# Kernel optimization log

Hardware: AMD Instinct MI355X
Metric: run time of the kernel (lower is better)

Reference implementation:

```python
import jax, jax.numpy as jnp
import numpy as np

B, S, DIM = 4, 2048, 768
H, HD, QK, R = 12, 64, 32, 8  # nheads, head_dim, qk_dim, nrules
EPS = 1e-5


def _ln(x, g, b):
    m = jnp.mean(x, axis=-1, keepdims=True)
    v = jnp.mean((x - m) ** 2, axis=-1, keepdims=True)
    return (x - m) / jnp.sqrt(v + EPS) * g + b


def setup_inputs() -> dict:
    key = jax.random.key(0)
    ks = jax.random.split(key, 12)
    w = lambda k, sh: (jax.random.normal(k, sh, jnp.float32) * 0.02)
    return {
        "x": jax.random.normal(ks[0], (B, S, DIM), jnp.float32),
        "Wq": w(ks[1], (DIM, DIM)), "bq": jnp.zeros((DIM,), jnp.float32),
        "Wk": w(ks[2], (DIM, DIM)), "bk": jnp.zeros((DIM,), jnp.float32),
        "Wv": w(ks[3], (DIM, HD * R)), "bv": jnp.zeros((HD * R,), jnp.float32),
        "Wqv": w(ks[4], (DIM, QK * H)), "bqv": jnp.zeros((QK * H,), jnp.float32),
        "Ws": w(ks[5], (QK + HD, 1)), "bs": jnp.zeros((1,), jnp.float32),
        "Wf": w(ks[6], (DIM, DIM)), "bf": jnp.zeros((DIM,), jnp.float32),
        "W1": w(ks[7], (DIM, 2 * DIM)), "b1": jnp.zeros((2 * DIM,), jnp.float32),
        "W2": w(ks[8], (2 * DIM, DIM)), "b2": jnp.zeros((DIM,), jnp.float32),
        "g1": jnp.ones((DIM,), jnp.float32), "be1": jnp.zeros((DIM,), jnp.float32),
        "g2": jnp.ones((DIM,), jnp.float32), "be2": jnp.zeros((DIM,), jnp.float32),
    }


def reference(x, Wq, bq, Wk, bk, Wv, bv, Wqv, bqv, Ws, bs, Wf, bf,
              W1, b1, W2, b2, g1, be1, g2, be2):
    b, n, _ = x.shape
    res = x
    xn = _ln(x, g1, be1)  # norm_before=True

    # --- stage 1: standard per-head attention, shared across rules ---
    q = (xn @ Wq + bq).reshape(b, n, H, HD) / np.sqrt(HD)
    k = (xn @ Wk + bk).reshape(b, n, H, HD)
    v = (xn @ Wv + bv).reshape(b, n, R, HD)
    score = jax.nn.softmax(jnp.einsum("bqhd,bkhd->bhqk", q, k), axis=-1)
    out = jnp.einsum("bhqk,bkrd->bqhrd", score, v)  # [B,S,H,R,hd]

    # --- stage 2: rule composition via score_network (dot=False) ---
    qv = (xn @ Wqv + bqv).reshape(b, n, H, QK) / np.sqrt(QK)
    # score_network(cat(q_v, out)) == q_v @ Ws[:QK] + out @ Ws[QK:] + bs
    ws_q, ws_o = Ws[:QK, 0], Ws[QK:, 0]
    comp = (jnp.einsum("bqhrd,d->bqhr", out, ws_o)
            + jnp.einsum("bqhk,k->bqh", qv, ws_q)[..., None] + bs[0])
    prev = comp[..., None]  # [B,S,H,R,1] raw scores, returned as `prev`

    rule_w = jax.nn.softmax(comp, axis=-1)  # softmax over rules
    o = jnp.einsum("bqhr,bqhrd->bqhd", rule_w, out).reshape(b, n, DIM)
    o = o @ Wf + bf

    out1 = res + o
    # post-block MLP (dropout inactive at inference)
    on = _ln(out1, g2, be2)
    mlp = jax.nn.relu(on @ W1 + b1) @ W2 + b2
    return out1 + mlp, prev
```

## Files before the change

kernel.cpp:

```cpp
#include <hip/hip_runtime.h>
#include <hip/hip_bf16.h>

typedef __bf16 bfrag  __attribute__((ext_vector_type(8)));
typedef __bf16 bf16x4 __attribute__((ext_vector_type(4)));
typedef float  f32x4  __attribute__((ext_vector_type(4)));

#define MFMA(a,b,c) __builtin_amdgcn_mfma_f32_16x16x32_bf16(a,b,c,0,0,0)

__device__ __forceinline__ void gl_lds16(const void* g, void* l) {
  __builtin_amdgcn_global_load_lds((const __attribute__((address_space(1))) void*)g,
                                   (__attribute__((address_space(3))) void*)l, 16, 0, 0);
}
__device__ __forceinline__ float fexp2(float x) {
  float r;
  asm("v_exp_f32 %0, %1" : "=v"(r) : "v"(x));
  return r;
}
__device__ __forceinline__ unsigned cvtpk(float lo, float hi) {
  unsigned r;
  asm("v_cvt_pk_bf16_f32 %0, %1, %2" : "=v"(r) : "v"(lo), "v"(hi));
  return r;
}

#define NC 2432

#define OFF_C     ((size_t)0)
#define OFF_VT    ((size_t)52428800)
#define OFF_QDOT  ((size_t)61079552)
#define OFF_WCAT  ((size_t)61472768)
#define OFF_BCAT  ((size_t)65208320)
#define OFF_WFT   ((size_t)65218048)
#define OFF_W1T   ((size_t)66397696)
#define OFF_W2T   ((size_t)68756992)
#define OFF_ATTNO ((size_t)71116288)
#define OFF_XN    ((size_t)39845888)
#define OFF_OUT1  ((size_t)0)
#define OFF_ON    ((size_t)12582912)
#define OFF_H1    ((size_t)25165824)

template<typename TIN>
__global__ __launch_bounds__(256) void k_ln(const TIN* __restrict__ in,
    const float* __restrict__ g, const float* __restrict__ be, __bf16* __restrict__ out) {
  int row  = blockIdx.x * 4 + (threadIdx.x >> 6);
  int lane = threadIdx.x & 63;
  const TIN* rp = in + (size_t)row * 768;
  float v[12];
  #pragma unroll
  for (int i = 0; i < 3; i++) {
    int c = i * 256 + lane * 4;
    if constexpr (sizeof(TIN) == 4) {
      float4 lv = *(const float4*)(rp + c);
      v[i*4+0] = lv.x; v[i*4+1] = lv.y; v[i*4+2] = lv.z; v[i*4+3] = lv.w;
    } else {
      bf16x4 lv = *(const bf16x4*)(rp + c);
      #pragma unroll
      for (int jj = 0; jj < 4; jj++) v[i*4+jj] = (float)lv[jj];
    }
  }
  float s = 0.f, sq = 0.f;
  #pragma unroll
  for (int k = 0; k < 12; k++) { s += v[k]; sq += v[k]*v[k]; }
  #pragma unroll
  for (int d = 1; d < 64; d <<= 1) { s += __shfl_xor(s, d); sq += __shfl_xor(sq, d); }
  float mean = s * (1.f/768.f);
  float rstd = rsqrtf(sq * (1.f/768.f) - mean*mean + 1e-5f);
  #pragma unroll
  for (int i = 0; i < 3; i++) {
    int c = i * 256 + lane * 4;
    float4 gv = *(const float4*)(g + c);
    float4 bv = *(const float4*)(be + c);
    bf16x4 o;
    o[0] = (__bf16)((v[i*4+0]-mean)*rstd*gv.x + bv.x);
    o[1] = (__bf16)((v[i*4+1]-mean)*rstd*gv.y + bv.y);
    o[2] = (__bf16)((v[i*4+2]-mean)*rstd*gv.z + bv.z);
    o[3] = (__bf16)((v[i*4+3]-mean)*rstd*gv.w + bv.w);
    *(bf16x4*)(out + (size_t)row*768 + c) = o;
  }
}

__global__ __launch_bounds__(256) void k_packT(const float* __restrict__ src, __bf16* __restrict__ dst,
                                               int N, int K, int total) {
  int idx = blockIdx.x * 256 + threadIdx.x;
  if (idx >= total) return;
  int K8 = K >> 3;
  int n = idx / K8, k0 = (idx % K8) * 8;
  bfrag o;
  #pragma unroll
  for (int i = 0; i < 8; i++) o[i] = (__bf16)src[(size_t)(k0+i)*N + n];
  *(bfrag*)&dst[(size_t)n*K + k0] = o;
}

__global__ __launch_bounds__(256) void k_packcat(
    const float* __restrict__ Wq, const float* __restrict__ Wk,
    const float* __restrict__ Wv, const float* __restrict__ Wqv,
    const float* __restrict__ bq, const float* __restrict__ bk,
    const float* __restrict__ bv, const float* __restrict__ bqv,
    __bf16* __restrict__ Wt, float* __restrict__ bcat) {
  int idx = blockIdx.x * 256 + threadIdx.x;
  if (idx >= 2432 * 96) return;
  int n = idx / 96, k0 = (idx % 96) * 8;
  const float* src; int col, sN; float sc = 1.f;
  if (n < 768)       { src = Wq;  col = n;        sN = 768; sc = 0.125f; }
  else if (n < 1536) { src = Wk;  col = n - 768;  sN = 768; }
  else if (n < 2048) { src = Wv;  col = n - 1536; sN = 512; }
  else               { src = Wqv; col = n - 2048; sN = 384; sc = 0.1767766952966369f; }
  bfrag o;
  #pragma unroll
  for (int i = 0; i < 8; i++) o[i] = (__bf16)(src[(size_t)(k0+i)*sN + col] * sc);
  *(bfrag*)&Wt[(size_t)n*768 + k0] = o;
  if (k0 == 0) {
    float bb;
    if (n < 768) bb = bq[col]*0.125f;
    else if (n < 1536) bb = bk[col];
    else if (n < 2048) bb = bv[col];
    else bb = bqv[col]*0.1767766952966369f;
    bcat[n] = bb;
  }
}

template<int KD, int EPI>
__global__ __launch_bounds__(256, 3) void k_gemm(const __bf16* __restrict__ A,
    const __bf16* __restrict__ Bt, const float* __restrict__ bias,
    const float* __restrict__ resf, const __bf16* __restrict__ resb,
    void* __restrict__ Cout, int N) {
  __shared__ __bf16 Al[2][128*32];
  __shared__ __bf16 Bl[2][128*32];
  const int bx = (blockIdx.x & 7) * 8 + (blockIdx.x >> 3);
  const int m0 = bx * 128, n0 = blockIdx.y * 128;
  const int tid = threadIdx.x, lane = tid & 63, w = tid >> 6;
  const int wm = (w >> 1) * 64, wn = (w & 1) * 64;
  const int srow = lane >> 2, skoff = (lane & 3) * 8;
  const int l15 = lane & 15, lg = lane >> 4;
  f32x4 acc[4][4];
  #pragma unroll
  for (int i = 0; i < 4; i++)
    #pragma unroll
    for (int j = 0; j < 4; j++) acc[i][j] = (f32x4){0.f,0.f,0.f,0.f};
  const int NT = KD / 32;
  auto stage = [&](int buf, int k0) {
    #pragma unroll
    for (int i = 0; i < 2; i++) {
      int c = w * 2 + i;
      gl_lds16(A  + (size_t)(m0 + c*16 + srow) * KD + k0 + skoff, &Al[buf][c*512]);
      gl_lds16(Bt + (size_t)(n0 + c*16 + srow) * KD + k0 + skoff, &Bl[buf][c*512]);
    }
  };
  stage(0, 0);
  __syncthreads();
  for (int t = 0; t < NT; t++) {
    int buf = t & 1;
    if (t + 1 < NT) stage(buf ^ 1, (t + 1) * 32);
    bfrag af[4], bfm[4];
    #pragma unroll
    for (int f = 0; f < 4; f++) {
      af[f]  = *(const bfrag*)&Al[buf][(wm + f*16 + l15)*32 + lg*8];
      bfm[f] = *(const bfrag*)&Bl[buf][(wn + f*16 + l15)*32 + lg*8];
    }
    #pragma unroll
    for (int i = 0; i < 4; i++)
      #pragma unroll
      for (int j = 0; j < 4; j++)
        acc[i][j] = MFMA(af[i], bfm[j], acc[i][j]);
    __syncthreads();
  }
  #pragma unroll
  for (int i = 0; i < 4; i++) {
    int row0 = m0 + wm + i*16 + lg*4;
    #pragma unroll
    for (int j = 0; j < 4; j++) {
      int col = n0 + wn + j*16 + l15;
      float bv = bias[col];
      #pragma unroll
      for (int q = 0; q < 4; q++) {
        size_t r = (size_t)(row0 + q);
        float v = acc[i][j][q] + bv;
        if (EPI == 0)      ((__bf16*)Cout)[r*N + col] = (__bf16)v;
        else if (EPI == 1) { v += resf[r*N + col]; ((__bf16*)Cout)[r*N + col] = (__bf16)v; }
        else if (EPI == 2) ((__bf16*)Cout)[r*N + col] = (__bf16)fmaxf(v, 0.f);
        else               { v += (float)resb[r*N + col]; ((float*)Cout)[r*N + col] = v; }
      }
    }
  }
}

__global__ __launch_bounds__(256) void k_vt(const __bf16* __restrict__ C, __bf16* __restrict__ VT) {
  int bid = blockIdx.x;
  int b = bid >> 8, dt = (bid >> 5) & 7, kt = bid & 31;
  __shared__ __bf16 tile[64][72];
  int tid = threadIdx.x;
  int r = tid >> 3, c0 = (tid & 7) * 8;
  #pragma unroll
  for (int p = 0; p < 2; p++) {
    int rr = r + p * 32;
    bfrag v = *(const bfrag*)&C[(size_t)(b*2048 + kt*64 + rr)*NC + 1536 + dt*64 + c0];
    *(bfrag*)&tile[rr][c0] = v;
  }
  __syncthreads();
  #pragma unroll
  for (int p = 0; p < 2; p++) {
    int d = r + p * 32;
    bfrag o;
    #pragma unroll
    for (int i = 0; i < 8; i++) o[i] = tile[c0 + i][d];
    *(bfrag*)&VT[((size_t)b*512 + dt*64 + d)*2048 + kt*64 + c0] = o;
  }
}

__global__ __launch_bounds__(256) void k_qdot(const __bf16* __restrict__ C, const float* __restrict__ Ws,
                                              const float* __restrict__ bs, float* __restrict__ qd) {
  int idx = blockIdx.x * 256 + threadIdx.x;
  if (idx >= 98304) return;
  int h = idx % 12; size_t srow = (size_t)(idx / 12);
  const __bf16* qp = &C[srow*NC + 2048 + h*32];
  float s = bs[0];
  #pragma unroll
  for (int j = 0; j < 32; j++) s += (float)qp[j] * Ws[j];
  qd[idx] = s;
}

__global__ __launch_bounds__(512, 2) void k_attn(const __bf16* __restrict__ C,
    const __bf16* __restrict__ VT, const float* __restrict__ Ws,
    const float* __restrict__ qdot, __bf16* __restrict__ attno, float* __restrict__ prevout) {
  __shared__ __align__(16) char smem[53248];
  __bf16* Pl   = (__bf16*)(smem);
  __bf16* kbuf = (__bf16*)(smem + 32768);
  float*  wlb  = (float*)(smem + 49152);
  __bf16* rbuf = (__bf16*)(smem);

  const int tid = threadIdx.x, lane = tid & 63, wid = tid >> 6;
  const int l15 = lane & 15, lg = lane >> 4;
  const int bid = (blockIdx.x & 7) * 96 + (blockIdx.x >> 3);
  const int b = bid / 192, rem = bid % 192, h = rem / 16, qb = rem % 16;
  const int q0 = qb * 128;

  const __bf16* VTb = VT + (size_t)b * 512 * 2048;
  const int kkey = tid >> 3, kch = tid & 7;
  const __bf16* Ksrc0 = C + (size_t)(b*2048 + kkey)*NC + 768 + h*64 + ((kch ^ (kkey & 7)) * 8);

  auto stageK = [&](int t) {
    gl_lds16(Ksrc0 + (size_t)t * 64 * NC, kbuf + (t & 1)*4096 + (size_t)wid*512);
  };
  stageK(0);

  const __bf16* Qbase = C + (size_t)(b*2048 + q0 + wid*16 + l15)*NC + h*64 + lg*8;
  bfrag qf0 = *(const bfrag*)(Qbase);
  bfrag qf1 = *(const bfrag*)(Qbase + 32);

  f32x4 accv[8][4];
  #pragma unroll
  for (int i = 0; i < 8; i++)
    #pragma unroll
    for (int j = 0; j < 4; j++) accv[i][j] = (f32x4){0.f,0.f,0.f,0.f};
  float lsc = 0.f;

  auto qk_phase = [&](int tn) {
    const __bf16* kb_ = kbuf + (tn & 1) * 4096;
    f32x4 s[4];
    #pragma unroll
    for (int cf = 0; cf < 4; cf++) s[cf] = (f32x4){0.f,0.f,0.f,0.f};
    #pragma unroll
    for (int cf = 0; cf < 4; cf++) {
      int key = cf*16 + l15, swz = key & 7;
      bfrag ka  = *(const bfrag*)(kb_ + key*64 + ((lg     ^ swz) * 8));
      bfrag kb2 = *(const bfrag*)(kb_ + key*64 + (((lg+4) ^ swz) * 8));
      s[cf] = MFMA(ka, qf0, s[cf]);
      s[cf] = MFMA(kb2, qf1, s[cf]);
    }
    int row = wid*16 + l15;
    char* base = (char*)Pl + (tn & 1)*16384 + row*128;
    int swz = (row & 7) << 4;
    #pragma unroll
    for (int cf = 0; cf < 4; cf++) {
      float p0 = fexp2(s[cf][0] * 1.44269504f);
      float p1 = fexp2(s[cf][1] * 1.44269504f);
      float p2 = fexp2(s[cf][2] * 1.44269504f);
      float p3 = fexp2(s[cf][3] * 1.44269504f);
      lsc += (p0 + p1) + (p2 + p3);
      uint2 pk;
      pk.x = cvtpk(p0, p1);
      pk.y = cvtpk(p2, p3);
      *(uint2*)(base + ((cf*32 + lg*8) ^ swz)) = pk;
    }
  };

  __syncthreads();

  qk_phase(0);
  stageK(1);

  for (int t = 0; t < 32; t++) {
    const int k0 = t * 64, pb = t & 1;
    __syncthreads();
    if (t + 2 < 32) stageK(t + 2);
    bfrag vb[4][2];
    #pragma unroll
    for (int cf = 0; cf < 4; cf++) {
      const __bf16* vp = VTb + (size_t)(wid*64 + cf*16 + l15)*2048 + k0 + lg*8;
      vb[cf][0] = *(const bfrag*)(vp);
      vb[cf][1] = *(const bfrag*)(vp + 32);
    }
    if (t < 31) qk_phase(t + 1);
    __builtin_amdgcn_s_setprio(1);
    #pragma unroll
    for (int rf = 0; rf < 8; rf++) {
      int prow = rf*16 + l15;
      int swz = (prow & 7) << 4;
      const char* pbase = (const char*)Pl + pb*16384 + prow*128;
      bfrag pa0 = *(const bfrag*)(pbase + ((lg*16) ^ swz));
      bfrag pa1 = *(const bfrag*)(pbase + ((64 + lg*16) ^ swz));
      #pragma unroll
      for (int cf = 0; cf < 4; cf++) {
        accv[rf][cf] = MFMA(pa0, vb[cf][0], accv[rf][cf]);
        accv[rf][cf] = MFMA(pa1, vb[cf][1], accv[rf][cf]);
      }
    }
    __builtin_amdgcn_s_setprio(0);
  }
  float lfall = lsc;
  lfall += __shfl_xor(lfall, 16);
  lfall += __shfl_xor(lfall, 32);
  float lf[4];
  #pragma unroll
  for (int j = 0; j < 4; j++) lf[j] = __shfl(lfall, lg*4 + j);

  {
    float wso = Ws[32 + l15];
    float wso1 = Ws[32 + 16 + l15];
    float wso2 = Ws[32 + 32 + l15];
    float wso3 = Ws[32 + 48 + l15];
    #pragma unroll
    for (int rf = 0; rf < 8; rf++) {
      #pragma unroll
      for (int j = 0; j < 4; j++) {
        float cj = accv[rf][0][j]*wso + accv[rf][1][j]*wso1
                 + accv[rf][2][j]*wso2 + accv[rf][3][j]*wso3;
        cj += __shfl_xor(cj, 1); cj += __shfl_xor(cj, 2);
        cj += __shfl_xor(cj, 4); cj += __shfl_xor(cj, 8);
        if (l15 == 0) wlb[(rf*16 + lg*4 + j)*8 + wid] = cj;
      }
    }
  }
  __syncthreads();
  {
    int rowg = b*2048 + q0 + wid*16 + lg*4;
    float cmp[4];
    #pragma unroll
    for (int j = 0; j < 4; j++) {
      float qdv = qdot[(size_t)(rowg + j)*12 + h];
      float cv = (l15 < 8) ? wlb[(wid*16 + lg*4 + j)*8 + l15] : 0.f;
      cmp[j] = (l15 < 8) ? (cv / lf[j] + qdv) : -INFINITY;
      if (l15 < 8) prevout[((size_t)(rowg + j)*12 + h)*8 + l15] = cmp[j];
    }
    #pragma unroll
    for (int j = 0; j < 4; j++) {
      float rm = cmp[j];
      rm = fmaxf(rm, __shfl_xor(rm, 1));
      rm = fmaxf(rm, __shfl_xor(rm, 2));
      rm = fmaxf(rm, __shfl_xor(rm, 4));
      float e = exp2f((cmp[j] - rm) * 1.44269504f);
      float rs = e;
      rs += __shfl_xor(rs, 1); rs += __shfl_xor(rs, 2); rs += __shfl_xor(rs, 4);
      float wp = e / (rs * lf[j]);
      if (l15 < 8) wlb[(wid*16 + lg*4 + j)*8 + l15] = wp;
    }
  }
  __syncthreads();
  #pragma unroll
  for (int c = 0; c < 4; c++) {
    #pragma unroll
    for (int rr = 0; rr < 2; rr++) {
      int rf = c*2 + rr;
      #pragma unroll
      for (int j = 0; j < 4; j++) {
        int row = rf*16 + lg*4 + j;
        int lrow = row - c*32;
        float wp = wlb[row*8 + wid];
        #pragma unroll
        for (int cf = 0; cf < 4; cf++)
          rbuf[((size_t)wid*32 + lrow)*64 + cf*16 + l15] = (__bf16)(accv[rf][cf][j] * wp);
      }
    }
    __syncthreads();
    {
      int row32 = tid >> 4, dc = (tid & 15) * 4;
      float os[4] = {0,0,0,0};
      #pragma unroll
      for (int r = 0; r < 8; r++) {
        bf16x4 v = *(const bf16x4*)&rbuf[((size_t)r*32 + row32)*64 + dc];
        #pragma unroll
        for (int i = 0; i < 4; i++) os[i] += (float)v[i];
      }
      int grow = c*32 + row32;
      bf16x4 ov;
      #pragma unroll
      for (int i = 0; i < 4; i++) ov[i] = (__bf16)os[i];
      *(bf16x4*)&attno[(size_t)(b*2048 + q0 + grow)*768 + h*64 + dc] = ov;
    }
    if (c < 3) __syncthreads();
  }
}

extern "C" void kernel_launch(void* const* d_in, const int* in_sizes, int n_in,
                              void* d_out, int out_size, void* d_ws, size_t ws_size,
                              hipStream_t stream) {
  (void)in_sizes; (void)n_in; (void)out_size; (void)ws_size;
  const float* x   = (const float*)d_in[0];
  const float* Wq  = (const float*)d_in[1];
  const float* bq  = (const float*)d_in[2];
  const float* Wk  = (const float*)d_in[3];
  const float* bk  = (const float*)d_in[4];
  const float* Wv  = (const float*)d_in[5];
  const float* bv  = (const float*)d_in[6];
  const float* Wqv = (const float*)d_in[7];
  const float* bqv = (const float*)d_in[8];
  const float* Ws  = (const float*)d_in[9];
  const float* bs  = (const float*)d_in[10];
  const float* Wf  = (const float*)d_in[11];
  const float* bfp = (const float*)d_in[12];
  const float* W1  = (const float*)d_in[13];
  const float* b1  = (const float*)d_in[14];
  const float* W2  = (const float*)d_in[15];
  const float* b2  = (const float*)d_in[16];
  const float* g1  = (const float*)d_in[17];
  const float* be1 = (const float*)d_in[18];
  const float* g2  = (const float*)d_in[19];
  const float* be2 = (const float*)d_in[20];

  char* ws = (char*)d_ws;
  __bf16* Cbuf  = (__bf16*)(ws + OFF_C);
  __bf16* xn    = (__bf16*)(ws + OFF_XN);
  __bf16* VTb   = (__bf16*)(ws + OFF_VT);
  float*  qdotb = (float*)(ws + OFF_QDOT);
  __bf16* Wcat  = (__bf16*)(ws + OFF_WCAT);
  float*  bcat  = (float*)(ws + OFF_BCAT);
  __bf16* WfT   = (__bf16*)(ws + OFF_WFT);
  __bf16* W1T   = (__bf16*)(ws + OFF_W1T);
  __bf16* W2T   = (__bf16*)(ws + OFF_W2T);
  __bf16* attno = (__bf16*)(ws + OFF_ATTNO);
  __bf16* out1  = (__bf16*)(ws + OFF_OUT1);
  __bf16* onb   = (__bf16*)(ws + OFF_ON);
  __bf16* h1    = (__bf16*)(ws + OFF_H1);
  float*  outp  = (float*)d_out;
  float*  prevp = outp + 6291456;

  k_ln<float><<<2048, 256, 0, stream>>>(x, g1, be1, xn);
  k_packcat<<<(2432*96 + 255)/256, 256, 0, stream>>>(Wq, Wk, Wv, Wqv, bq, bk, bv, bqv, Wcat, bcat);
  k_packT<<<(768*96 + 255)/256, 256, 0, stream>>>(Wf, WfT, 768, 768, 768*96);
  k_packT<<<(1536*96 + 255)/256, 256, 0, stream>>>(W1, W1T, 1536, 768, 1536*96);
  k_packT<<<(768*192 + 255)/256, 256, 0, stream>>>(W2, W2T, 768, 1536, 768*192);

  k_gemm<768, 0><<<dim3(64, 19), 256, 0, stream>>>(xn, Wcat, bcat, nullptr, nullptr, Cbuf, NC);

  k_vt<<<1024, 256, 0, stream>>>(Cbuf, VTb);
  k_qdot<<<384, 256, 0, stream>>>(Cbuf, Ws, bs, qdotb);

  k_attn<<<768, 512, 0, stream>>>(Cbuf, VTb, Ws, qdotb, attno, prevp);

  k_gemm<768, 1><<<dim3(64, 6), 256, 0, stream>>>(attno, WfT, bfp, x, nullptr, out1, 768);
  k_ln<__bf16><<<2048, 256, 0, stream>>>(out1, g2, be2, onb);
  k_gemm<768, 2><<<dim3(64, 12), 256, 0, stream>>>(onb, W1T, b1, nullptr, nullptr, h1, 1536);
  k_gemm<1536, 3><<<dim3(64, 6), 256, 0, stream>>>(h1, W2T, b2, nullptr, out1, outp, 768);
}
```

Measured before the change: 501.2 us.

## Merge weight-packing kernels, fold qdot into V transpose, drop setprio

Result: faster. 480.7 us (-4.1%).

```diff
diff --git a/kernel.cpp b/kernel.cpp
--- a/kernel.cpp
+++ b/kernel.cpp
@@ -78,10 +78,8 @@
   }
 }
 
-__global__ __launch_bounds__(256) void k_packT(const float* __restrict__ src, __bf16* __restrict__ dst,
-                                               int N, int K, int total) {
-  int idx = blockIdx.x * 256 + threadIdx.x;
-  if (idx >= total) return;
+__device__ __forceinline__ void packT_body(const float* __restrict__ src, __bf16* __restrict__ dst,
+                                           int N, int K, int idx) {
   int K8 = K >> 3;
   int n = idx / K8, k0 = (idx % K8) * 8;
   bfrag o;
@@ -90,31 +88,45 @@
   *(bfrag*)&dst[(size_t)n*K + k0] = o;
 }
 
-__global__ __launch_bounds__(256) void k_packcat(
+__global__ __launch_bounds__(256) void k_packall(
     const float* __restrict__ Wq, const float* __restrict__ Wk,
     const float* __restrict__ Wv, const float* __restrict__ Wqv,
     const float* __restrict__ bq, const float* __restrict__ bk,
     const float* __restrict__ bv, const float* __restrict__ bqv,
-    __bf16* __restrict__ Wt, float* __restrict__ bcat) {
-  int idx = blockIdx.x * 256 + threadIdx.x;
-  if (idx >= 2432 * 96) return;
-  int n = idx / 96, k0 = (idx % 96) * 8;
-  const float* src; int col, sN; float sc = 1.f;
-  if (n < 768)       { src = Wq;  col = n;        sN = 768; sc = 0.125f; }
-  else if (n < 1536) { src = Wk;  col = n - 768;  sN = 768; }
-  else if (n < 2048) { src = Wv;  col = n - 1536; sN = 512; }
-  else               { src = Wqv; col = n - 2048; sN = 384; sc = 0.1767766952966369f; }
-  bfrag o;
-  #pragma unroll
-  for (int i = 0; i < 8; i++) o[i] = (__bf16)(src[(size_t)(k0+i)*sN + col] * sc);
-  *(bfrag*)&Wt[(size_t)n*768 + k0] = o;
-  if (k0 == 0) {
-    float bb;
-    if (n < 768) bb = bq[col]*0.125f;
-    else if (n < 1536) bb = bk[col];
-    else if (n < 2048) bb = bv[col];
-    else bb = bqv[col]*0.1767766952966369f;
-    bcat[n] = bb;
+    const float* __restrict__ Wf, const float* __restrict__ W1, const float* __restrict__ W2,
+    __bf16* __restrict__ Wcat, float* __restrict__ bcat,
+    __bf16* __restrict__ WfT, __bf16* __restrict__ W1T, __bf16* __restrict__ W2T) {
+  int bidx = blockIdx.x;
+  if (bidx < 912) {
+    int idx = bidx * 256 + threadIdx.x;
+    if (idx >= 2432 * 96) return;
+    int n = idx / 96, k0 = (idx % 96) * 8;
+    const float* src; int col, sN; float sc = 1.f;
+    if (n < 768)       { src = Wq;  col = n;        sN = 768; sc = 0.125f; }
+    else if (n < 1536) { src = Wk;  col = n - 768;  sN = 768; }
+    else if (n < 2048) { src = Wv;  col = n - 1536; sN = 512; }
+    else               { src = Wqv; col = n - 2048; sN = 384; sc = 0.1767766952966369f; }
+    bfrag o;
+    #pragma unroll
+    for (int i = 0; i < 8; i++) o[i] = (__bf16)(src[(size_t)(k0+i)*sN + col] * sc);
+    *(bfrag*)&Wcat[(size_t)n*768 + k0] = o;
+    if (k0 == 0) {
+      float bb;
+      if (n < 768) bb = bq[col]*0.125f;
+      else if (n < 1536) bb = bk[col];
+      else if (n < 2048) bb = bv[col];
+      else bb = bqv[col]*0.1767766952966369f;
+      bcat[n] = bb;
+    }
+  } else if (bidx < 1200) {
+    int idx = (bidx - 912) * 256 + threadIdx.x;
+    if (idx < 768*96) packT_body(Wf, WfT, 768, 768, idx);
+  } else if (bidx < 1776) {
+    int idx = (bidx - 1200) * 256 + threadIdx.x;
+    if (idx < 1536*96) packT_body(W1, W1T, 1536, 768, idx);
+  } else {
+    int idx = (bidx - 1776) * 256 + threadIdx.x;
+    if (idx < 768*192) packT_body(W2, W2T, 768, 1536, idx);
   }
 }
 
@@ -183,7 +195,9 @@
   }
 }
 
-__global__ __launch_bounds__(256) void k_vt(const __bf16* __restrict__ C, __bf16* __restrict__ VT) {
+__global__ __launch_bounds__(256) void k_vt(const __bf16* __restrict__ C, const float* __restrict__ Ws,
+                                            const float* __restrict__ bs,
+                                            __bf16* __restrict__ VT, float* __restrict__ qd) {
   int bid = blockIdx.x;
   int b = bid >> 8, dt = (bid >> 5) & 7, kt = bid & 31;
   __shared__ __bf16 tile[64][72];
@@ -204,18 +218,24 @@
     for (int i = 0; i < 8; i++) o[i] = tile[c0 + i][d];
     *(bfrag*)&VT[((size_t)b*512 + dt*64 + d)*2048 + kt*64 + c0] = o;
   }
-}
-
-__global__ __launch_bounds__(256) void k_qdot(const __bf16* __restrict__ C, const float* __restrict__ Ws,
-                                              const float* __restrict__ bs, float* __restrict__ qd) {
-  int idx = blockIdx.x * 256 + threadIdx.x;
-  if (idx >= 98304) return;
-  int h = idx % 12; size_t srow = (size_t)(idx / 12);
-  const __bf16* qp = &C[srow*NC + 2048 + h*32];
-  float s = bs[0];
-  #pragma unroll
-  for (int j = 0; j < 32; j++) s += (float)qp[j] * Ws[j];
-  qd[idx] = s;
+  if (dt == 0) {
+    float bsv = bs[0];
+    #pragma unroll
+    for (int p = 0; p < 3; p++) {
+      int idx = p * 256 + tid;
+      int rl = idx / 12, h = idx % 12;
+      size_t srow = (size_t)(b*2048 + kt*64 + rl);
+      const __bf16* qp = &C[srow*NC + 2048 + h*32];
+      float s = bsv;
+      #pragma unroll
+      for (int c = 0; c < 4; c++) {
+        bfrag v = *(const bfrag*)(qp + c*8);
+        #pragma unroll
+        for (int i = 0; i < 8; i++) s += (float)v[i] * Ws[c*8 + i];
+      }
+      qd[srow*12 + h] = s;
+    }
+  }
 }
 
 __global__ __launch_bounds__(512, 2) void k_attn(const __bf16* __restrict__ C,
@@ -300,7 +320,6 @@
       vb[cf][1] = *(const bfrag*)(vp + 32);
     }
     if (t < 31) qk_phase(t + 1);
-    __builtin_amdgcn_s_setprio(1);
     #pragma unroll
     for (int rf = 0; rf < 8; rf++) {
       int prow = rf*16 + l15;
@@ -314,7 +333,6 @@
         accv[rf][cf] = MFMA(pa1, vb[cf][1], accv[rf][cf]);
       }
     }
-    __builtin_amdgcn_s_setprio(0);
   }
   float lfall = lsc;
   lfall += __shfl_xor(lfall, 16);
@@ -444,15 +462,12 @@
   float*  prevp = outp + 6291456;
 
   k_ln<float><<<2048, 256, 0, stream>>>(x, g1, be1, xn);
-  k_packcat<<<(2432*96 + 255)/256, 256, 0, stream>>>(Wq, Wk, Wv, Wqv, bq, bk, bv, bqv, Wcat, bcat);
-  k_packT<<<(768*96 + 255)/256, 256, 0, stream>>>(Wf, WfT, 768, 768, 768*96);
-  k_packT<<<(1536*96 + 255)/256, 256, 0, stream>>>(W1, W1T, 1536, 768, 1536*96);
-  k_packT<<<(768*192 + 255)/256, 256, 0, stream>>>(W2, W2T, 768, 1536, 768*192);
+  k_packall<<<2352, 256, 0, stream>>>(Wq, Wk, Wv, Wqv, bq, bk, bv, bqv,
+                                      Wf, W1, W2, Wcat, bcat, WfT, W1T, W2T);
 
   k_gemm<768, 0><<<dim3(64, 19), 256, 0, stream>>>(xn, Wcat, bcat, nullptr, nullptr, Cbuf, NC);
 
-  k_vt<<<1024, 256, 0, stream>>>(Cbuf, VTb);
-  k_qdot<<<384, 256, 0, stream>>>(Cbuf, Ws, bs, qdotb);
+  k_vt<<<1024, 256, 0, stream>>>(Cbuf, Ws, bs, VTb, qdotb);
 
   k_attn<<<768, 512, 0, stream>>>(Cbuf, VTb, Ws, qdotb, attno, prevp);
 
```
